# Performance work log

Measured on AMD Instinct MI355X. Metric: run time of the kernel, lower is better.

Reference implementation:

```python
import jax, jax.numpy as jnp
import numpy as np

HIDDEN = 2048
EXPERTS = 8
INTER = 1024
TOP_K = 2
AUX_LOSS_WEIGHT = 0.01
TOKENS = 8192


def setup_inputs() -> dict:
    key = jax.random.key(0)
    k_x, k_g, k_w1, k_w2 = jax.random.split(key, 4)
    x = jax.random.normal(k_x, (TOKENS, HIDDEN), dtype=jnp.float32)
    # nn.Linear(hidden, experts, bias=False): weight is [E, H], applied as x @ W^T
    gate_w = jax.random.normal(k_g, (EXPERTS, HIDDEN), dtype=jnp.float32) * 0.02
    w1 = jax.random.normal(k_w1, (EXPERTS, HIDDEN, INTER), dtype=jnp.float32) * 0.02
    w2 = jax.random.normal(k_w2, (EXPERTS, INTER, HIDDEN), dtype=jnp.float32) * 0.02
    return {"x": x, "gate_w": gate_w, "w1": w1, "w2": w2}


def _moe_forward(x, gate_w, w1, w2):
    E = gate_w.shape[0]
    logits = x @ gate_w.T                              # [T, E]
    probs = jax.nn.softmax(logits, axis=-1)            # [T, E]
    topk_w, topk_idx = jax.lax.top_k(probs, TOP_K)     # [T, K]
    topk_w = topk_w / jnp.sum(topk_w, axis=-1, keepdims=True)

    # load-balancing aux loss: E * sum_e f_e * P_e
    one_hot = jax.nn.one_hot(topk_idx, E, dtype=probs.dtype)   # [T, K, E]
    f = jnp.mean(jnp.sum(one_hot, axis=1), axis=0)             # fraction of tokens per expert
    P = jnp.mean(probs, axis=0)                                # mean router prob per expert
    aux_loss = AUX_LOSS_WEIGHT * E * jnp.sum(f * P)

    # grouped expert MLP (dense-over-experts formulation, same math as
    # permute -> grouped GEMM -> unpermute):
    h = jnp.einsum('th,ehi->tei', x, w1)               # [T, E, I]
    h = jax.nn.gelu(h)
    y = jnp.einsum('tei,eih->teh', h, w2)              # [T, E, H]

    # combine: gather each token's top-k expert outputs and weight them
    y_sel = jnp.take_along_axis(y, topk_idx[:, :, None], axis=1)  # [T, K, H]
    out = jnp.sum(y_sel * topk_w[:, :, None], axis=1)             # [T, H]
    return out, aux_loss


def reference(x, gate_w, w1, w2):
    return _moe_forward(x, gate_w, w1, w2)
```

## Files before the change

### kernel.cpp

```cpp
#include <hip/hip_runtime.h>
#include <hip/hip_fp16.h>
#include <cmath>

#define T_TOKENS 8192
#define HID 2048
#define NEXP 8
#define INTERM 1024
#define GATE_NB 2048
#define MAX_TT 136
#define GEMM_NB 512

typedef _Float16 f16x8 __attribute__((ext_vector_type(8)));
typedef _Float16 f16x4 __attribute__((ext_vector_type(4)));
typedef float f32x4 __attribute__((ext_vector_type(4)));

static __device__ __forceinline__ float gelu_tanh(float v) {
    return 0.5f * v * (1.0f + tanhf(0.79788456080286535588f * (v + 0.044715f * v * v * v)));
}

static __device__ __forceinline__ void glds16(const void* g, void* l) {
    __builtin_amdgcn_global_load_lds((const __attribute__((address_space(1))) void*)g,
                                     (__attribute__((address_space(3))) void*)l, 16, 0, 0);
}

static __device__ __forceinline__ f16x8 lds_read(const _Float16* base, int row, int chunk) {
    int phys = chunk ^ (row & 7);
    return *reinterpret_cast<const f16x8*>(
        reinterpret_cast<const char*>(base) + row * 128 + phys * 16);
}

__global__ __launch_bounds__(256) void tconv_kernel(const float* __restrict__ in,
                                                    _Float16* __restrict__ out,
                                                    int R, int C) {
    __shared__ float t[32][33];
    int z = blockIdx.z;
    int r0 = blockIdx.y * 32, c0 = blockIdx.x * 32;
    int tid = threadIdx.x;
    int r = tid >> 3, c4 = (tid & 7) * 4;
    const float4 v = *reinterpret_cast<const float4*>(&in[((size_t)z * R + (r0 + r)) * C + c0 + c4]);
    t[r][c4 + 0] = v.x; t[r][c4 + 1] = v.y; t[r][c4 + 2] = v.z; t[r][c4 + 3] = v.w;
    __syncthreads();
    int oc = tid >> 3;
    int or4 = (tid & 7) * 4;
    f16x4 o;
    o[0] = (_Float16)t[or4 + 0][oc];
    o[1] = (_Float16)t[or4 + 1][oc];
    o[2] = (_Float16)t[or4 + 2][oc];
    o[3] = (_Float16)t[or4 + 3][oc];
    *reinterpret_cast<f16x4*>(&out[((size_t)z * C + (c0 + oc)) * R + r0 + or4]) = o;
}

__global__ __launch_bounds__(256) void gate_kernel(const float* __restrict__ x,
                                                   const float* __restrict__ gw,
                                                   _Float16* __restrict__ xh,
                                                   int* __restrict__ tk_idx, float* __restrict__ tk_w,
                                                   int* __restrict__ part_cnt,
                                                   double* __restrict__ part_sumP) {
    __shared__ double sds[4][NEXP];
    __shared__ int sci[4][NEXP];
    int w = threadIdx.x >> 6;
    int lane = threadIdx.x & 63;
    int t = blockIdx.x * 4 + w;

    const float4* xr = (const float4*)(x + (size_t)t * HID);
    _Float16* xo = xh + (size_t)t * HID;
    double acc[NEXP];
#pragma unroll
    for (int e = 0; e < NEXP; e++) acc[e] = 0.0;
#pragma unroll
    for (int i = 0; i < HID / 256; i++) {
        float4 xv = xr[i * 64 + lane];
        f16x4 h;
        h[0] = (_Float16)xv.x; h[1] = (_Float16)xv.y;
        h[2] = (_Float16)xv.z; h[3] = (_Float16)xv.w;
        *reinterpret_cast<f16x4*>(xo + i * 256 + lane * 4) = h;
#pragma unroll
        for (int e = 0; e < NEXP; e++) {
            float4 gv = ((const float4*)(gw + (size_t)e * HID))[i * 64 + lane];
            acc[e] += (double)xv.x * (double)gv.x + (double)xv.y * (double)gv.y
                    + (double)xv.z * (double)gv.z + (double)xv.w * (double)gv.w;
        }
    }
#pragma unroll
    for (int e = 0; e < NEXP; e++) {
#pragma unroll
        for (int off = 32; off > 0; off >>= 1) acc[e] += __shfl_xor(acc[e], off, 64);
    }
    double mx = acc[0];
#pragma unroll
    for (int e = 1; e < NEXP; e++) mx = acc[e] > mx ? acc[e] : mx;
    double ex[NEXP];
    double sum = 0.0;
#pragma unroll
    for (int e = 0; e < NEXP; e++) { ex[e] = exp(acc[e] - mx); sum += ex[e]; }
    int i0 = 0;
#pragma unroll
    for (int e = 1; e < NEXP; e++) if (ex[e] > ex[i0]) i0 = e;
    int i1 = (i0 == 0) ? 1 : 0;
#pragma unroll
    for (int e = 0; e < NEXP; e++) if (e != i0 && ex[e] > ex[i1]) i1 = e;
    double p0 = ex[i0], p1 = ex[i1];
    double t2 = p0 + p1;
    if (lane == 0) {
        tk_idx[2 * t] = i0; tk_idx[2 * t + 1] = i1;
        tk_w[2 * t] = (float)(p0 / t2); tk_w[2 * t + 1] = (float)(p1 / t2);
#pragma unroll
        for (int e = 0; e < NEXP; e++) {
            sds[w][e] = ex[e] / sum;
            sci[w][e] = (e == i0 ? 1 : 0) + (e == i1 ? 1 : 0);
        }
    }
    __syncthreads();
    if (threadIdx.x < NEXP) {
        int e = threadIdx.x;
        part_sumP[e * GATE_NB + blockIdx.x] = sds[0][e] + sds[1][e] + sds[2][e] + sds[3][e];
        part_cnt[e * GATE_NB + blockIdx.x]  = sci[0][e] + sci[1][e] + sci[2][e] + sci[3][e];
    }
}

__global__ __launch_bounds__(256) void finalize_kernel(const int* __restrict__ part_cnt,
                                                       const double* __restrict__ part_sumP,
                                                       int* __restrict__ cnt, int* __restrict__ offs,
                                                       int* __restrict__ cursor,
                                                       int* __restrict__ ttab,
                                                       int* __restrict__ nmt,
                                                       int* __restrict__ steal,
                                                       float* __restrict__ aux_out) {
    __shared__ double swv[4];
    __shared__ int cwv[4];
    __shared__ double sE[NEXP];
    __shared__ int cE[NEXP];
    int w = threadIdx.x >> 6;
    int lane = threadIdx.x & 63;
    for (int e = 0; e < NEXP; e++) {
        double s = 0.0; int c = 0;
        for (int j = threadIdx.x; j < GATE_NB; j += 256) {
            s += part_sumP[e * GATE_NB + j];
            c += part_cnt[e * GATE_NB + j];
        }
#pragma unroll
        for (int off = 32; off > 0; off >>= 1) {
            s += __shfl_xor(s, off, 64);
            c += __shfl_xor(c, off, 64);
        }
        if (lane == 0) { swv[w] = s; cwv[w] = c; }
        __syncthreads();
        if (threadIdx.x == 0) {
            sE[e] = swv[0] + swv[1] + swv[2] + swv[3];
            cE[e] = cwv[0] + cwv[1] + cwv[2] + cwv[3];
        }
        __syncthreads();
    }
    if (threadIdx.x == 0) {
        int off = 0;
        double aux = 0.0;
        int idx = 0;
#pragma unroll
        for (int e = 0; e < NEXP; e++) {
            cnt[e] = cE[e];
            offs[e] = off;
            off += cE[e];
            cursor[e] = 0;
            aux += ((double)cE[e] / (double)T_TOKENS) * (sE[e] / (double)T_TOKENS);
            int mt = (cE[e] + 127) >> 7;
            for (int m = 0; m < mt; m++) ttab[idx++] = (e << 16) | m;
        }
        nmt[0] = idx;
        for (; idx < MAX_TT; idx++) ttab[idx] = -1;
        for (int i = 0; i < 16; i++) steal[i] = 0;
        aux_out[0] = (float)(0.01 * (double)NEXP * aux);
    }
}

__global__ void scatter_kernel(const int* __restrict__ tk_idx, const float* __restrict__ tk_w,
                               const int* __restrict__ offs, int* __restrict__ cursor,
                               int* __restrict__ row_tok, float* __restrict__ row_w,
                               int* __restrict__ tok_row) {
    int t = blockIdx.x * blockDim.x + threadIdx.x;
    int lane = threadIdx.x & 63;
    unsigned long long below = (lane == 0) ? 0ull : ((~0ull) >> (64 - lane));
    for (int k = 0; k < 2; k++) {
        int e = tk_idx[2 * t + k];
        float wv = tk_w[2 * t + k];
        int pos = 0;
#pragma unroll
        for (int ee = 0; ee < NEXP; ee++) {
            unsigned long long m = __ballot(e == ee);
            if (e == ee) {
                int rank = (int)__popcll(m & below);
                int leader = (int)__ffsll((unsigned long long)m) - 1;
                int b = 0;
                if (lane == leader) b = atomicAdd(&cursor[ee], (int)__popcll(m));
                b = __shfl(b, leader, 64);
                pos = b + rank;
            }
        }
        int r = offs[e] + pos;
        row_tok[r] = t;
        row_w[r] = wv;
        tok_row[2 * t + k] = r;
    }
}

template<bool GATHER, bool GELU, int KTOT, int NX>
__global__ __launch_bounds__(256, 2) void gemm8_kernel(
    const _Float16* __restrict__ Aglob,
    const _Float16* __restrict__ Bglob,
    const int* __restrict__ cnt, const int* __restrict__ offs,
    const int* __restrict__ row_tok,
    const int* __restrict__ ttab,
    const int* __restrict__ nmt,
    int* __restrict__ steal,
    _Float16* __restrict__ Out, int Ncols)
{
    constexpr int NT = KTOT / 64;
    __shared__ __align__(16) _Float16 As[2][128][64];
    __shared__ __align__(16) _Float16 Bs[2][128][64];
    __shared__ int s_it;

    int tid = threadIdx.x;
    int w = tid >> 6, lane = tid & 63;
    int wr = w >> 1, wc = w & 1;
    int fr = lane & 15, fq = lane >> 4;

    int n_items = nmt[0] * NX;
    int chunk = (n_items + 7) >> 3;
    int xcd = blockIdx.x & 7;

    int srow = tid >> 3;
    int lc = (tid & 7) ^ (srow & 7);

    _Float16* ldsA = &As[0][0][0] + w * 512;
    _Float16* ldsB = &Bs[0][0][0] + w * 512;

    for (;;) {
        __syncthreads();
        if (tid == 0) s_it = atomicAdd(&steal[xcd], 1);
        __syncthreads();
        int i = s_it;
        if (i >= chunk) break;
        int it = xcd * chunk + i;
        if (it >= n_items) break;

        int ent = ttab[it / NX];
        int e = ent >> 16;
        int m0 = (ent & 0xffff) << 7;
        int Ne = cnt[e];
        int base = offs[e];
        int n0 = (it & (NX - 1)) << 7;

        const _Float16* aS[4];
#pragma unroll
        for (int r = 0; r < 4; r++) {
            int ar = m0 + r * 32 + srow; if (ar >= Ne) ar = Ne - 1;
            int id = GATHER ? row_tok[base + ar] : (base + ar);
            aS[r] = Aglob + (size_t)id * KTOT + lc * 8;
        }
        const size_t bexp = (size_t)e * Ncols * KTOT;
        const _Float16* bS[4];
#pragma unroll
        for (int r = 0; r < 4; r++)
            bS[r] = Bglob + bexp + (size_t)(n0 + r * 32 + srow) * KTOT + lc * 8;

#define STAGE(S, KOFF) do {                                         \
        glds16(aS[0] + (KOFF), ldsA + (S) * 8192 + 0 * 2048);       \
        glds16(aS[1] + (KOFF), ldsA + (S) * 8192 + 1 * 2048);       \
        glds16(aS[2] + (KOFF), ldsA + (S) * 8192 + 2 * 2048);       \
        glds16(aS[3] + (KOFF), ldsA + (S) * 8192 + 3 * 2048);       \
        glds16(bS[0] + (KOFF), ldsB + (S) * 8192 + 0 * 2048);       \
        glds16(bS[1] + (KOFF), ldsB + (S) * 8192 + 1 * 2048);       \
        glds16(bS[2] + (KOFF), ldsB + (S) * 8192 + 2 * 2048);       \
        glds16(bS[3] + (KOFF), ldsB + (S) * 8192 + 3 * 2048);       \
    } while (0)

        f32x4 acc[4][4] = {};
        STAGE(0, 0);

        for (int j = 0; j < NT; ++j) {
            int slot = j & 1;
            const _Float16* Ab = &As[slot][0][0];
            const _Float16* Bb = &Bs[slot][0][0];
            if (j + 1 < NT) {
                STAGE(slot ^ 1, (j + 1) * 64);
                asm volatile("s_waitcnt vmcnt(8)" ::: "memory");
            } else {
                asm volatile("s_waitcnt vmcnt(0)" ::: "memory");
            }
            __builtin_amdgcn_s_barrier();

            f16x8 b_[4][2];
            {
                f16x8 a_[2][2];
#pragma unroll
                for (int i2 = 0; i2 < 2; i2++)
#pragma unroll
                    for (int k = 0; k < 2; k++)
                        a_[i2][k] = lds_read(Ab, wr * 64 + i2 * 16 + fr, k * 4 + fq);
#pragma unroll
                for (int jj = 0; jj < 4; jj++)
#pragma unroll
                    for (int k = 0; k < 2; k++)
                        b_[jj][k] = lds_read(Bb, wc * 64 + jj * 16 + fr, k * 4 + fq);
                asm volatile("s_waitcnt lgkmcnt(0)" ::: "memory");
                __builtin_amdgcn_s_setprio(1);
#pragma unroll
                for (int i2 = 0; i2 < 2; i2++)
#pragma unroll
                    for (int jj = 0; jj < 4; jj++)
#pragma unroll
                        for (int k = 0; k < 2; k++)
                            acc[i2][jj] = __builtin_amdgcn_mfma_f32_16x16x32_f16(
                                a_[i2][k], b_[jj][k], acc[i2][jj], 0, 0, 0);
                __builtin_amdgcn_s_setprio(0);
            }
            {
                f16x8 a_[2][2];
#pragma unroll
                for (int i2 = 0; i2 < 2; i2++)
#pragma unroll
                    for (int k = 0; k < 2; k++)
                        a_[i2][k] = lds_read(Ab, wr * 64 + (2 + i2) * 16 + fr, k * 4 + fq);
                asm volatile("s_waitcnt lgkmcnt(0)" ::: "memory");
                __builtin_amdgcn_s_setprio(1);
#pragma unroll
                for (int i2 = 0; i2 < 2; i2++)
#pragma unroll
                    for (int jj = 0; jj < 4; jj++)
#pragma unroll
                        for (int k = 0; k < 2; k++)
                            acc[2 + i2][jj] = __builtin_amdgcn_mfma_f32_16x16x32_f16(
                                a_[i2][k], b_[jj][k], acc[2 + i2][jj], 0, 0, 0);
                __builtin_amdgcn_s_setprio(0);
            }
            __builtin_amdgcn_s_barrier();
        }
#undef STAGE

#pragma unroll
        for (int mi = 0; mi < 4; mi++) {
#pragma unroll
            for (int r = 0; r < 4; r++) {
                int row = m0 + wr * 64 + mi * 16 + fq * 4 + r;
                if (row < Ne) {
                    _Float16* dst = Out + (size_t)(base + row) * Ncols + n0 + wc * 64 + fr;
#pragma unroll
                    for (int ni = 0; ni < 4; ni++) {
                        float v = acc[mi][ni][r];
                        if (GELU) v = gelu_tanh(v);
                        dst[ni * 16] = (_Float16)v;
                    }
                }
            }
        }
    }
}

__global__ __launch_bounds__(256) void combine_kernel(const _Float16* __restrict__ y,
                                                      const int* __restrict__ tok_row,
                                                      const float* __restrict__ tk_w,
                                                      float* __restrict__ out) {
    int t = blockIdx.x;
    int c = threadIdx.x;
    int r0 = tok_row[2 * t], r1 = tok_row[2 * t + 1];
    float w0 = tk_w[2 * t], w1 = tk_w[2 * t + 1];
    f16x8 a = reinterpret_cast<const f16x8*>(y + (size_t)r0 * HID)[c];
    f16x8 b = reinterpret_cast<const f16x8*>(y + (size_t)r1 * HID)[c];
    float4 o0, o1;
    o0.x = w0 * (float)a[0] + w1 * (float)b[0];
    o0.y = w0 * (float)a[1] + w1 * (float)b[1];
    o0.z = w0 * (float)a[2] + w1 * (float)b[2];
    o0.w = w0 * (float)a[3] + w1 * (float)b[3];
    o1.x = w0 * (float)a[4] + w1 * (float)b[4];
    o1.y = w0 * (float)a[5] + w1 * (float)b[5];
    o1.z = w0 * (float)a[6] + w1 * (float)b[6];
    o1.w = w0 * (float)a[7] + w1 * (float)b[7];
    float4* dst = reinterpret_cast<float4*>(out + (size_t)t * HID + c * 8);
    dst[0] = o0;
    dst[1] = o1;
}

extern "C" void kernel_launch(void* const* d_in, const int* in_sizes, int n_in,
                              void* d_out, int out_size, void* d_ws, size_t ws_size,
                              hipStream_t stream) {
    const float* x  = (const float*)d_in[0];
    const float* gw = (const float*)d_in[1];
    const float* w1 = (const float*)d_in[2];
    const float* w2 = (const float*)d_in[3];
    float* out = (float*)d_out;
    char* ws = (char*)d_ws;

    int*    cnt       = (int*)(ws + 0);
    int*    cursor    = (int*)(ws + 64);
    int*    offs      = (int*)(ws + 128);
    int*    nmt       = (int*)(ws + 256);
    int*    steal     = (int*)(ws + 320);
    int*    ttab      = (int*)(ws + 512);
    int*    part_cnt  = (int*)(ws + 4096);
    double* part_sumP = (double*)(ws + 131072);
    int*    row_tok   = (int*)(ws + 262144);
    float*  row_w     = (float*)(ws + 327680);
    int*    tk_idx    = (int*)(ws + 393216);
    float*  tk_w      = (float*)(ws + 458752);
    int*    tok_row   = (int*)(ws + 524288);
    const size_t OFF = 589824;
    _Float16* xh  = (_Float16*)(ws + OFF);
    _Float16* w1t = (_Float16*)(ws + OFF + (1ull << 25));
    _Float16* w2t = (_Float16*)(ws + OFF + (2ull << 25));
    _Float16* hh  = (_Float16*)(ws + OFF + (3ull << 25));
    _Float16* y   = (_Float16*)(ws + OFF);

    dim3 g1(INTERM / 32, HID / 32, NEXP);
    tconv_kernel<<<g1, 256, 0, stream>>>(w1, w1t, HID, INTERM);
    dim3 g2(HID / 32, INTERM / 32, NEXP);
    tconv_kernel<<<g2, 256, 0, stream>>>(w2, w2t, INTERM, HID);

    gate_kernel<<<GATE_NB, 256, 0, stream>>>(x, gw, xh, tk_idx, tk_w, part_cnt, part_sumP);
    finalize_kernel<<<1, 256, 0, stream>>>(part_cnt, part_sumP, cnt, offs, cursor, ttab,
                                           nmt, steal, out + (size_t)T_TOKENS * HID);
    scatter_kernel<<<T_TOKENS / 256, 256, 0, stream>>>(tk_idx, tk_w, offs, cursor,
                                                       row_tok, row_w, tok_row);

    gemm8_kernel<true, true, HID, INTERM / 128>
        <<<GEMM_NB, 256, 0, stream>>>(xh, w1t, cnt, offs, row_tok, ttab, nmt, steal, hh, INTERM);
    gemm8_kernel<false, false, INTERM, HID / 128>
        <<<GEMM_NB, 256, 0, stream>>>(hh, w2t, cnt, offs, row_tok, ttab, nmt, steal + 8, y, HID);

    combine_kernel<<<T_TOKENS, 256, 0, stream>>>(y, tok_row, tk_w, out);
}
```

Measured before the change: 411.5 us.

## Use 256x256-tile 512-thread GEMM for down projection and merge prep kernels

Replaces the second expert GEMM with a new kernel that uses 256x256 output tiles, 8 waves, double-buffered direct-to-LDS loads and MFMA phases, driven by a new 256-row tile table built in finalize. It also merges the two weight transpose kernels and the gate kernel into one launch with block-index dispatch. The larger tile aims to raise operand reuse and cut global traffic for the H=2048 output GEMM. The launch merge removes launch gaps. In exchange, tiles are more heavily padded for experts with uneven counts, and there are fewer blocks to balance across CUs.

```diff
diff --git a/kernel.cpp b/kernel.cpp
--- a/kernel.cpp
+++ b/kernel.cpp
@@ -8,7 +8,9 @@
 #define INTERM 1024
 #define GATE_NB 2048
 #define MAX_TT 136
+#define MAX_TT2 72
 #define GEMM_NB 512
+#define GEMM2_NB 256
 
 typedef _Float16 f16x8 __attribute__((ext_vector_type(8)));
 typedef _Float16 f16x4 __attribute__((ext_vector_type(4)));
@@ -29,15 +31,14 @@
         reinterpret_cast<const char*>(base) + row * 128 + phys * 16);
 }
 
-__global__ __launch_bounds__(256) void tconv_kernel(const float* __restrict__ in,
-                                                    _Float16* __restrict__ out,
-                                                    int R, int C) {
+static __device__ __forceinline__ void tconv_body(const float* __restrict__ in,
+                                                  _Float16* __restrict__ out,
+                                                  int R, int C, int bx, int by, int bz) {
     __shared__ float t[32][33];
-    int z = blockIdx.z;
-    int r0 = blockIdx.y * 32, c0 = blockIdx.x * 32;
+    int r0 = by * 32, c0 = bx * 32;
     int tid = threadIdx.x;
     int r = tid >> 3, c4 = (tid & 7) * 4;
-    const float4 v = *reinterpret_cast<const float4*>(&in[((size_t)z * R + (r0 + r)) * C + c0 + c4]);
+    const float4 v = *reinterpret_cast<const float4*>(&in[((size_t)bz * R + (r0 + r)) * C + c0 + c4]);
     t[r][c4 + 0] = v.x; t[r][c4 + 1] = v.y; t[r][c4 + 2] = v.z; t[r][c4 + 3] = v.w;
     __syncthreads();
     int oc = tid >> 3;
@@ -47,20 +48,20 @@
     o[1] = (_Float16)t[or4 + 1][oc];
     o[2] = (_Float16)t[or4 + 2][oc];
     o[3] = (_Float16)t[or4 + 3][oc];
-    *reinterpret_cast<f16x4*>(&out[((size_t)z * C + (c0 + oc)) * R + r0 + or4]) = o;
-}
-
-__global__ __launch_bounds__(256) void gate_kernel(const float* __restrict__ x,
-                                                   const float* __restrict__ gw,
-                                                   _Float16* __restrict__ xh,
-                                                   int* __restrict__ tk_idx, float* __restrict__ tk_w,
-                                                   int* __restrict__ part_cnt,
-                                                   double* __restrict__ part_sumP) {
+    *reinterpret_cast<f16x4*>(&out[((size_t)bz * C + (c0 + oc)) * R + r0 + or4]) = o;
+}
+
+static __device__ __forceinline__ void gate_body(const float* __restrict__ x,
+                                                 const float* __restrict__ gw,
+                                                 _Float16* __restrict__ xh,
+                                                 int* __restrict__ tk_idx, float* __restrict__ tk_w,
+                                                 int* __restrict__ part_cnt,
+                                                 double* __restrict__ part_sumP, int gid) {
     __shared__ double sds[4][NEXP];
     __shared__ int sci[4][NEXP];
     int w = threadIdx.x >> 6;
     int lane = threadIdx.x & 63;
-    int t = blockIdx.x * 4 + w;
+    int t = gid * 4 + w;
 
     const float4* xr = (const float4*)(x + (size_t)t * HID);
     _Float16* xo = xh + (size_t)t * HID;
@@ -113,8 +114,31 @@
     __syncthreads();
     if (threadIdx.x < NEXP) {
         int e = threadIdx.x;
-        part_sumP[e * GATE_NB + blockIdx.x] = sds[0][e] + sds[1][e] + sds[2][e] + sds[3][e];
-        part_cnt[e * GATE_NB + blockIdx.x]  = sci[0][e] + sci[1][e] + sci[2][e] + sci[3][e];
+        part_sumP[e * GATE_NB + gid] = sds[0][e] + sds[1][e] + sds[2][e] + sds[3][e];
+        part_cnt[e * GATE_NB + gid]  = sci[0][e] + sci[1][e] + sci[2][e] + sci[3][e];
+    }
+}
+
+__global__ __launch_bounds__(256) void prep_kernel(const float* __restrict__ x,
+                                                   const float* __restrict__ gw,
+                                                   const float* __restrict__ w1,
+                                                   const float* __restrict__ w2,
+                                                   _Float16* __restrict__ xh,
+                                                   _Float16* __restrict__ w1t,
+                                                   _Float16* __restrict__ w2t,
+                                                   int* __restrict__ tk_idx, float* __restrict__ tk_w,
+                                                   int* __restrict__ part_cnt,
+                                                   double* __restrict__ part_sumP) {
+    int bid = blockIdx.x;
+    if (bid < 16384) {
+        int bx = bid & 31, by = (bid >> 5) & 63, bz = bid >> 11;
+        tconv_body(w1, w1t, HID, INTERM, bx, by, bz);
+    } else if (bid < 32768) {
+        int r = bid - 16384;
+        int bx = r & 63, by = (r >> 6) & 31, bz = r >> 11;
+        tconv_body(w2, w2t, INTERM, HID, bx, by, bz);
+    } else {
+        gate_body(x, gw, xh, tk_idx, tk_w, part_cnt, part_sumP, bid - 32768);
     }
 }
 
@@ -123,6 +147,7 @@
                                                        int* __restrict__ cnt, int* __restrict__ offs,
                                                        int* __restrict__ cursor,
                                                        int* __restrict__ ttab,
+                                                       int* __restrict__ ttab2,
                                                        int* __restrict__ nmt,
                                                        int* __restrict__ steal,
                                                        float* __restrict__ aux_out) {
@@ -154,7 +179,7 @@
     if (threadIdx.x == 0) {
         int off = 0;
         double aux = 0.0;
-        int idx = 0;
+        int idx = 0, idx2 = 0;
 #pragma unroll
         for (int e = 0; e < NEXP; e++) {
             cnt[e] = cE[e];
@@ -164,9 +189,13 @@
             aux += ((double)cE[e] / (double)T_TOKENS) * (sE[e] / (double)T_TOKENS);
             int mt = (cE[e] + 127) >> 7;
             for (int m = 0; m < mt; m++) ttab[idx++] = (e << 16) | m;
+            int mt2 = (cE[e] + 255) >> 8;
+            for (int m = 0; m < mt2; m++) ttab2[idx2++] = (e << 16) | m;
         }
         nmt[0] = idx;
+        nmt[1] = idx2;
         for (; idx < MAX_TT; idx++) ttab[idx] = -1;
+        for (; idx2 < MAX_TT2; idx2++) ttab2[idx2] = -1;
         for (int i = 0; i < 16; i++) steal[i] = 0;
         aux_out[0] = (float)(0.01 * (double)NEXP * aux);
     }
@@ -349,6 +378,184 @@
                         if (GELU) v = gelu_tanh(v);
                         dst[ni * 16] = (_Float16)v;
                     }
+                }
+            }
+        }
+    }
+}
+
+template<int KTOT, int NX>
+__global__ __launch_bounds__(512, 2) void gemm256_kernel(
+    const _Float16* __restrict__ Aglob,
+    const _Float16* __restrict__ Bglob,
+    const int* __restrict__ cnt, const int* __restrict__ offs,
+    const int* __restrict__ ttab2,
+    const int* __restrict__ nmt,
+    int* __restrict__ steal,
+    _Float16* __restrict__ Out, int Ncols)
+{
+    constexpr int NT = KTOT / 64;
+    __shared__ __align__(16) _Float16 As[2][256][64];
+    __shared__ __align__(16) _Float16 Bs[2][256][64];
+    __shared__ int s_it;
+
+    int tid = threadIdx.x;
+    int w = tid >> 6, lane = tid & 63;
+    int wr = w >> 2, wc = w & 3;
+    int fr = lane & 15, fq = lane >> 4;
+
+    int n_items = nmt[1] * NX;
+    int chunk = (n_items + 7) >> 3;
+    int xcd = blockIdx.x & 7;
+
+    int grow = lane >> 3;
+    int lc = (lane & 7) ^ grow;
+
+    _Float16* ldsA = &As[0][0][0] + (w * 32) * 64;
+    _Float16* ldsB = &Bs[0][0][0] + (w * 32) * 64;
+
+    for (;;) {
+        __syncthreads();
+        if (tid == 0) s_it = atomicAdd(&steal[xcd], 1);
+        __syncthreads();
+        int i = s_it;
+        if (i >= chunk) break;
+        int it = xcd * chunk + i;
+        if (it >= n_items) break;
+
+        int ent = ttab2[it / NX];
+        int e = ent >> 16;
+        int m0 = (ent & 0xffff) << 8;
+        int Ne = cnt[e];
+        int base = offs[e];
+        int n0 = (it & (NX - 1)) << 8;
+
+        const _Float16* aS[4];
+#pragma unroll
+        for (int g = 0; g < 4; g++) {
+            int ar = m0 + w * 32 + g * 8 + grow; if (ar >= Ne) ar = Ne - 1;
+            aS[g] = Aglob + (size_t)(base + ar) * KTOT + lc * 8;
+        }
+        const size_t bexp = (size_t)e * Ncols * KTOT;
+        const _Float16* bS[4];
+#pragma unroll
+        for (int g = 0; g < 4; g++)
+            bS[g] = Bglob + bexp + (size_t)(n0 + w * 32 + g * 8 + grow) * KTOT + lc * 8;
+
+        f32x4 acc[8][4] = {};
+
+#pragma unroll
+        for (int g = 0; g < 4; g++) glds16(aS[g], ldsA + g * 512);
+#pragma unroll
+        for (int g = 0; g < 4; g++) glds16(bS[g], ldsB + g * 512);
+
+        for (int j = 0; j < NT; ++j) {
+            int slot = j & 1;
+            const _Float16* Ab = &As[slot][0][0];
+            const _Float16* Bb = &Bs[slot][0][0];
+            _Float16* An = ldsA + (slot ^ 1) * 16384;
+            _Float16* Bn = ldsB + (slot ^ 1) * 16384;
+            int koff = (j + 1) * 64;
+            bool more = (j + 1 < NT);
+            if (more) {
+                glds16(aS[0] + koff, An + 0 * 512);
+                glds16(aS[1] + koff, An + 1 * 512);
+                asm volatile("s_waitcnt vmcnt(2)" ::: "memory");
+            } else {
+                asm volatile("s_waitcnt vmcnt(0)" ::: "memory");
+            }
+            __builtin_amdgcn_s_barrier();
+
+            f16x8 b_[4];
+            {
+                f16x8 a_[4];
+#pragma unroll
+                for (int i2 = 0; i2 < 4; i2++)
+                    a_[i2] = lds_read(Ab, wr * 128 + i2 * 16 + fr, fq);
+#pragma unroll
+                for (int jj = 0; jj < 4; jj++)
+                    b_[jj] = lds_read(Bb, wc * 64 + jj * 16 + fr, fq);
+                if (more) { glds16(aS[2] + koff, An + 2 * 512); glds16(aS[3] + koff, An + 3 * 512); }
+                __builtin_amdgcn_s_barrier();
+                asm volatile("s_waitcnt lgkmcnt(0)" ::: "memory");
+                __builtin_amdgcn_s_setprio(1);
+#pragma unroll
+                for (int i2 = 0; i2 < 4; i2++)
+#pragma unroll
+                    for (int jj = 0; jj < 4; jj++)
+                        acc[i2][jj] = __builtin_amdgcn_mfma_f32_16x16x32_f16(
+                            a_[i2], b_[jj], acc[i2][jj], 0, 0, 0);
+                __builtin_amdgcn_s_setprio(0);
+                __builtin_amdgcn_s_barrier();
+            }
+            {
+                f16x8 a_[4];
+#pragma unroll
+                for (int i2 = 0; i2 < 4; i2++)
+                    a_[i2] = lds_read(Ab, wr * 128 + (4 + i2) * 16 + fr, fq);
+                if (more) { glds16(bS[0] + koff, Bn + 0 * 512); glds16(bS[1] + koff, Bn + 1 * 512); }
+                __builtin_amdgcn_s_barrier();
+                asm volatile("s_waitcnt lgkmcnt(0)" ::: "memory");
+                __builtin_amdgcn_s_setprio(1);
+#pragma unroll
+                for (int i2 = 0; i2 < 4; i2++)
+#pragma unroll
+                    for (int jj = 0; jj < 4; jj++)
+                        acc[4 + i2][jj] = __builtin_amdgcn_mfma_f32_16x16x32_f16(
+                            a_[i2], b_[jj], acc[4 + i2][jj], 0, 0, 0);
+                __builtin_amdgcn_s_setprio(0);
+                __builtin_amdgcn_s_barrier();
+            }
+            {
+                f16x8 a_[4];
+#pragma unroll
+                for (int i2 = 0; i2 < 4; i2++)
+                    a_[i2] = lds_read(Ab, wr * 128 + i2 * 16 + fr, 4 + fq);
+#pragma unroll
+                for (int jj = 0; jj < 4; jj++)
+                    b_[jj] = lds_read(Bb, wc * 64 + jj * 16 + fr, 4 + fq);
+                if (more) { glds16(bS[2] + koff, Bn + 2 * 512); glds16(bS[3] + koff, Bn + 3 * 512); }
+                __builtin_amdgcn_s_barrier();
+                asm volatile("s_waitcnt lgkmcnt(0)" ::: "memory");
+                __builtin_amdgcn_s_setprio(1);
+#pragma unroll
+                for (int i2 = 0; i2 < 4; i2++)
+#pragma unroll
+                    for (int jj = 0; jj < 4; jj++)
+                        acc[i2][jj] = __builtin_amdgcn_mfma_f32_16x16x32_f16(
+                            a_[i2], b_[jj], acc[i2][jj], 0, 0, 0);
+                __builtin_amdgcn_s_setprio(0);
+                __builtin_amdgcn_s_barrier();
+            }
+            {
+                f16x8 a_[4];
+#pragma unroll
+                for (int i2 = 0; i2 < 4; i2++)
+                    a_[i2] = lds_read(Ab, wr * 128 + (4 + i2) * 16 + fr, 4 + fq);
+                __builtin_amdgcn_s_barrier();
+                asm volatile("s_waitcnt lgkmcnt(0)" ::: "memory");
+                __builtin_amdgcn_s_setprio(1);
+#pragma unroll
+                for (int i2 = 0; i2 < 4; i2++)
+#pragma unroll
+                    for (int jj = 0; jj < 4; jj++)
+                        acc[4 + i2][jj] = __builtin_amdgcn_mfma_f32_16x16x32_f16(
+                            a_[i2], b_[jj], acc[4 + i2][jj], 0, 0, 0);
+                __builtin_amdgcn_s_setprio(0);
+                __builtin_amdgcn_s_barrier();
+            }
+        }
+
+#pragma unroll
+        for (int mi = 0; mi < 8; mi++) {
+#pragma unroll
+            for (int r = 0; r < 4; r++) {
+                int row = m0 + wr * 128 + mi * 16 + fq * 4 + r;
+                if (row < Ne) {
+                    _Float16* dst = Out + (size_t)(base + row) * Ncols + n0 + wc * 64 + fr;
+#pragma unroll
+                    for (int ni = 0; ni < 4; ni++)
+                        dst[ni * 16] = (_Float16)acc[mi][ni][r];
                 }
             }
         }
@@ -395,6 +602,7 @@
     int*    nmt       = (int*)(ws + 256);
     int*    steal     = (int*)(ws + 320);
     int*    ttab      = (int*)(ws + 512);
+    int*    ttab2     = (int*)(ws + 2048);
     int*    part_cnt  = (int*)(ws + 4096);
     double* part_sumP = (double*)(ws + 131072);
     int*    row_tok   = (int*)(ws + 262144);
@@ -409,21 +617,18 @@
     _Float16* hh  = (_Float16*)(ws + OFF + (3ull << 25));
     _Float16* y   = (_Float16*)(ws + OFF);
 
-    dim3 g1(INTERM / 32, HID / 32, NEXP);
-    tconv_kernel<<<g1, 256, 0, stream>>>(w1, w1t, HID, INTERM);
-    dim3 g2(HID / 32, INTERM / 32, NEXP);
-    tconv_kernel<<<g2, 256, 0, stream>>>(w2, w2t, INTERM, HID);
-
-    gate_kernel<<<GATE_NB, 256, 0, stream>>>(x, gw, xh, tk_idx, tk_w, part_cnt, part_sumP);
-    finalize_kernel<<<1, 256, 0, stream>>>(part_cnt, part_sumP, cnt, offs, cursor, ttab,
-                                           nmt, steal, out + (size_t)T_TOKENS * HID);
+    prep_kernel<<<32768 + GATE_NB, 256, 0, stream>>>(x, gw, w1, w2, xh, w1t, w2t,
+                                                     tk_idx, tk_w, part_cnt, part_sumP);
+    finalize_kernel<<<1, 256, 0, stream>>>(part_cnt, part_sumP, cnt, offs, cursor,
+                                           ttab, ttab2, nmt, steal,
+                                           out + (size_t)T_TOKENS * HID);
     scatter_kernel<<<T_TOKENS / 256, 256, 0, stream>>>(tk_idx, tk_w, offs, cursor,
                                                        row_tok, row_w, tok_row);
 
     gemm8_kernel<true, true, HID, INTERM / 128>
         <<<GEMM_NB, 256, 0, stream>>>(xh, w1t, cnt, offs, row_tok, ttab, nmt, steal, hh, INTERM);
-    gemm8_kernel<false, false, INTERM, HID / 128>
-        <<<GEMM_NB, 256, 0, stream>>>(hh, w2t, cnt, offs, row_tok, ttab, nmt, steal + 8, y, HID);
+    gemm256_kernel<INTERM, HID / 256>
+        <<<GEMM2_NB, 512, 0, stream>>>(hh, w2t, cnt, offs, ttab2, nmt, steal + 8, y, HID);
 
     combine_kernel<<<T_TOKENS, 256, 0, stream>>>(y, tok_row, tk_w, out);
 }
```

After: 390.2 us. 1.05x faster.
